# Performance work log

Hardware: AMD Instinct MI355X
Metric: run time of the kernel (lower is better)

Reference implementation:

```python
import jax, jax.numpy as jnp
import numpy as np

VOCAB, D = 50000, 300
B, LC = 64, 32
T, LT = 256, 64
N_SENTS = 5


def setup_inputs() -> dict:
    key = jax.random.key(0)
    k1, k2, k3 = jax.random.split(key, 3)
    claim = jax.random.randint(k1, (B, LC), 0, VOCAB)
    targets = jax.random.randint(k2, (B, T, LT), 0, VOCAB)
    embeddings = jax.random.normal(k3, (VOCAB, D), dtype=jnp.float32)
    return {"claim": claim, "targets": targets, "embeddings": embeddings, "n": N_SENTS}


def reference(claim, targets, embeddings, n):
    # Embedding lookups (frozen table)
    c = embeddings[claim]          # [B, Lc, d]
    t = embeddings[targets]        # [B, T, Lt, d]
    # batch_U = claim[:,None] @ targets^T  -> [B, T, Lc, Lt]
    U = jnp.einsum('bcd,btld->btcl', c, t)
    # softmax over target tokens (axis=3), max over claim tokens (axis=2)
    sm = jax.nn.softmax(U, axis=3)
    scores = jnp.max(sm, axis=2)           # [B, T, Lt]
    target_scores = jnp.sum(scores, axis=2)  # [B, T]
    # per-batch top-n target sentences (sorted order; torch used sorted=False,
    # the selected set is identical)
    _, idx = jax.lax.top_k(target_scores, n)  # [B, n]
    top = jnp.take_along_axis(U, idx[:, :, None, None], axis=1)  # [B, n, Lc, Lt]
    # L2-normalize over last axis (torch dim=2 of the [n, Lc, Lt] slice)
    norm = jnp.sqrt(jnp.sum(top * top, axis=3, keepdims=True))
    return top / norm
```

## Files before the change

### kernel.cpp

```cpp
#include <hip/hip_runtime.h>
#include <hip/hip_bf16.h>

#define VOCAB 50000
#define D     300
#define B_    64
#define LC    32
#define T_    256
#define LT    64
#define NSEL  5

#define A_U4   2560
#define A_HALF 20480
#define TROW   640

typedef _Float16 half8_t __attribute__((ext_vector_type(8)));
typedef float    f32x4   __attribute__((ext_vector_type(4)));

__global__ __launch_bounds__(256) void k_prep(const int* __restrict__ claim,
                                              const float* __restrict__ emb,
                                              _Float16* __restrict__ tab,
                                              _Float16* __restrict__ wsA,
                                              int tableBlocks) {
    int wave = threadIdx.x >> 6, lane = threadIdx.x & 63;
    if ((int)blockIdx.x < tableBlocks) {
        int r = blockIdx.x * 4 + wave;
        const float* src = emb + (size_t)r * D;
        _Float16* d = tab + (size_t)r * TROW;
#pragma unroll
        for (int i = 0; i < 5; ++i) {
            int k = lane + i * 64;
            float x = (k < D) ? src[k] : 0.0f;
            _Float16 h = (_Float16)x;
            int blk = k >> 5, off = k & 31;
            d[blk * 64 + off]      = h;
            d[blk * 64 + 32 + off] = (_Float16)(x - (float)h);
        }
    } else {
        int row = (blockIdx.x - tableBlocks) * 4 + wave;
        int b = row >> 5, m = row & 31;
        int tok = claim[row];
        const float* src = emb + (size_t)tok * D;
        _Float16* base = wsA + (size_t)b * A_HALF;
#pragma unroll
        for (int i = 0; i < 5; ++i) {
            int k = lane + i * 64;
            float x = (k < D) ? src[k] : 0.0f;
            _Float16 h = (_Float16)x;
            int sp = ((k >> 3) ^ (m & 7));
            int idx = (m * 40 + sp) * 8 + (k & 7);
            base[idx] = h;
            base[10240 + idx] = (_Float16)(x - (float)h);
        }
    }
}

__device__ __forceinline__ void split8(const float4& a, const float4& b,
                                       half8_t& hv, half8_t& lv) {
    float x[8] = {a.x, a.y, a.z, a.w, b.x, b.y, b.z, b.w};
#pragma unroll
    for (int i = 0; i < 8; ++i) {
        _Float16 h = (_Float16)x[i];
        hv[i] = h;
        lv[i] = (_Float16)(x[i] - (float)h);
    }
}

template<bool FAST, int NI>
__device__ __forceinline__ void compute_U(const uint4* sA,
                                          const float* __restrict__ emb,
                                          const _Float16* __restrict__ tab,
                                          const int* __restrict__ trow, int lcol0,
                                          int lane, f32x4 acc[2][NI]) {
    int ln = lane & 15, quad = lane >> 4;
#pragma unroll
    for (int mi = 0; mi < 2; ++mi)
#pragma unroll
        for (int ni = 0; ni < NI; ++ni) acc[mi][ni] = (f32x4)0.0f;

    int arow0 = ln * 40;
    int arow1 = (16 + ln) * 40;
    int key = ln & 7;
    int qo = quad * 8;

    if (FAST) {
        const _Float16* rp[NI];
#pragma unroll
        for (int ni = 0; ni < NI; ++ni) {
            int tok = trow[lcol0 + ni * 16 + ln];
            rp[ni] = tab + (size_t)tok * TROW;
        }
        half8_t bh[2][NI], bl[2][NI];
#pragma unroll
        for (int ni = 0; ni < NI; ++ni) {
            bh[0][ni] = *(const half8_t*)(rp[ni] + qo);
            bl[0][ni] = *(const half8_t*)(rp[ni] + 32 + qo);
        }
#pragma unroll
        for (int ks = 0; ks < 10; ++ks) {
            int cur = ks & 1, nxt = cur ^ 1;
            if (ks < 9) {
                int ko = (ks + 1) * 64 + qo;
#pragma unroll
                for (int ni = 0; ni < NI; ++ni) {
                    bh[nxt][ni] = *(const half8_t*)(rp[ni] + ko);
                    bl[nxt][ni] = *(const half8_t*)(rp[ni] + 32 + ko);
                }
            }
            int sp = (ks * 4 + quad) ^ key;
            half8_t ah[2], al[2];
            ah[0] = __builtin_bit_cast(half8_t, sA[arow0 + sp]);
            al[0] = __builtin_bit_cast(half8_t, sA[1280 + arow0 + sp]);
            ah[1] = __builtin_bit_cast(half8_t, sA[arow1 + sp]);
            al[1] = __builtin_bit_cast(half8_t, sA[1280 + arow1 + sp]);
#pragma unroll
            for (int mi = 0; mi < 2; ++mi)
#pragma unroll
                for (int ni = 0; ni < NI; ++ni) {
                    acc[mi][ni] = __builtin_amdgcn_mfma_f32_16x16x32_f16(ah[mi], bh[cur][ni], acc[mi][ni], 0, 0, 0);
                    acc[mi][ni] = __builtin_amdgcn_mfma_f32_16x16x32_f16(ah[mi], bl[cur][ni], acc[mi][ni], 0, 0, 0);
                    acc[mi][ni] = __builtin_amdgcn_mfma_f32_16x16x32_f16(al[mi], bh[cur][ni], acc[mi][ni], 0, 0, 0);
                }
        }
    } else {
        const float* bp[NI];
#pragma unroll
        for (int ni = 0; ni < NI; ++ni) {
            int tok = trow[lcol0 + ni * 16 + ln];
            bp[ni] = emb + (size_t)tok * D;
        }
#pragma unroll 1
        for (int ks = 0; ks < 10; ++ks) {
            int kb = ks * 32 + qo;
            int ka = kb > 296 ? 296 : kb;
            int kb4 = kb + 4;
            int kbb = kb4 > 296 ? 296 : kb4;
            float4 b0[NI], b1[NI];
#pragma unroll
            for (int ni = 0; ni < NI; ++ni) {
                b0[ni] = *(const float4*)(bp[ni] + ka);
                b1[ni] = *(const float4*)(bp[ni] + kbb);
            }
            if (kb >= 296) {
                float4 z = make_float4(0.f, 0.f, 0.f, 0.f);
#pragma unroll
                for (int ni = 0; ni < NI; ++ni) {
                    if (kb >= 300) b0[ni] = z;
                    b1[ni] = z;
                }
            }
            int sp = (ks * 4 + quad) ^ key;
            half8_t ah[2], al[2];
            ah[0] = __builtin_bit_cast(half8_t, sA[arow0 + sp]);
            al[0] = __builtin_bit_cast(half8_t, sA[1280 + arow0 + sp]);
            ah[1] = __builtin_bit_cast(half8_t, sA[arow1 + sp]);
            al[1] = __builtin_bit_cast(half8_t, sA[1280 + arow1 + sp]);
            half8_t bh[NI], bl[NI];
#pragma unroll
            for (int ni = 0; ni < NI; ++ni) split8(b0[ni], b1[ni], bh[ni], bl[ni]);
#pragma unroll
            for (int mi = 0; mi < 2; ++mi)
#pragma unroll
                for (int ni = 0; ni < NI; ++ni) {
                    acc[mi][ni] = __builtin_amdgcn_mfma_f32_16x16x32_f16(ah[mi], bh[ni], acc[mi][ni], 0, 0, 0);
                    acc[mi][ni] = __builtin_amdgcn_mfma_f32_16x16x32_f16(ah[mi], bl[ni], acc[mi][ni], 0, 0, 0);
                    acc[mi][ni] = __builtin_amdgcn_mfma_f32_16x16x32_f16(al[mi], bh[ni], acc[mi][ni], 0, 0, 0);
                }
        }
    }
}

__device__ __forceinline__ float xmax4(float v) {
    v = fmaxf(v, __shfl_xor(v, 1)); v = fmaxf(v, __shfl_xor(v, 2));
    v = fmaxf(v, __shfl_xor(v, 4)); v = fmaxf(v, __shfl_xor(v, 8));
    return v;
}
__device__ __forceinline__ float xsum4(float v) {
    v += __shfl_xor(v, 1); v += __shfl_xor(v, 2);
    v += __shfl_xor(v, 4); v += __shfl_xor(v, 8);
    return v;
}

template<bool FAST>
__global__ __launch_bounds__(256, 4) void k_scores(const int* __restrict__ targets,
                                                   const float* __restrict__ emb,
                                                   const _Float16* __restrict__ tab,
                                                   const _Float16* __restrict__ wsA,
                                                   float* __restrict__ wsScr) {
    __shared__ __align__(16) uint4 sA[A_U4];
    int wg = blockIdx.x;
    int xcd = wg & 7, rest = wg >> 3;
    int b = xcd * 8 + (rest >> 6);
    int tg = rest & 63;
    int tid = threadIdx.x;
    {
        const uint4* src = (const uint4*)(wsA + (size_t)b * A_HALF);
        for (int i = tid; i < A_U4; i += 256) sA[i] = src[i];
    }
    __syncthreads();

    int lane = tid & 63, wave = tid >> 6;
    int t = tg * 4 + wave;
    const int* trow = targets + ((size_t)b * T_ + t) * LT;

    f32x4 acc[2][4];
    compute_U<FAST, 4>(sA, emb, tab, trow, 0, lane, acc);

    float score_l[4] = {0.f, 0.f, 0.f, 0.f};
#pragma unroll
    for (int mi = 0; mi < 2; ++mi)
#pragma unroll
        for (int r = 0; r < 4; ++r) {
            float m = fmaxf(fmaxf(acc[mi][0][r], acc[mi][1][r]),
                            fmaxf(acc[mi][2][r], acc[mi][3][r]));
            m = xmax4(m);
            float p[4], s = 0.f;
#pragma unroll
            for (int ni = 0; ni < 4; ++ni) { p[ni] = __expf(acc[mi][ni][r] - m); s += p[ni]; }
            s = xsum4(s);
            float rv = 1.0f / s;
#pragma unroll
            for (int ni = 0; ni < 4; ++ni) score_l[ni] = fmaxf(score_l[ni], p[ni] * rv);
        }
    float tot = 0.f;
#pragma unroll
    for (int ni = 0; ni < 4; ++ni) {
        float v = score_l[ni];
        v = fmaxf(v, __shfl_xor(v, 16));
        v = fmaxf(v, __shfl_xor(v, 32));
        tot += v;
    }
    tot = xsum4(tot);
    if (lane == 0) wsScr[b * T_ + t] = tot;
}

template<bool FAST>
__global__ __launch_bounds__(256) void k_output(const int* __restrict__ targets,
                                                const float* __restrict__ emb,
                                                const _Float16* __restrict__ tab,
                                                const _Float16* __restrict__ wsA,
                                                const float* __restrict__ wsScr,
                                                float* __restrict__ out) {
    __shared__ __align__(16) uint4 sA[A_U4];
    __shared__ float sS[LC][4];
    __shared__ int sT;
    int b = blockIdx.y, j = blockIdx.x, tid = threadIdx.x;
    int lane = tid & 63, wave = tid >> 6;
    if (wave) {
        const uint4* src = (const uint4*)(wsA + (size_t)b * A_HALF);
        for (int i = tid - 64; i < A_U4; i += 192) sA[i] = src[i];
    } else {
        float v[4];
#pragma unroll
        for (int i = 0; i < 4; ++i) v[i] = wsScr[b * T_ + lane + 64 * i];
        int sel = 0;
        for (int r = 0; r <= j; ++r) {
            float bv = v[0]; int bi = lane;
#pragma unroll
            for (int i = 1; i < 4; ++i) {
                int idx = lane + 64 * i;
                if (v[i] > bv) { bv = v[i]; bi = idx; }
            }
            for (int off = 32; off > 0; off >>= 1) {
                float ov = __shfl_down(bv, off);
                int   oi = __shfl_down(bi, off);
                if (ov > bv || (ov == bv && oi < bi)) { bv = ov; bi = oi; }
            }
            bi = __shfl(bi, 0);
            sel = bi;
            if ((bi & 63) == lane) v[bi >> 6] = -1e30f;
        }
        if (lane == 0) sT = sel;
    }
    __syncthreads();

    int t = sT;
    const int* trow = targets + ((size_t)b * T_ + t) * LT;
    f32x4 acc[2][1];
    compute_U<FAST, 1>(sA, emb, tab, trow, wave * 16, lane, acc);

    int ln = lane & 15, quad = lane >> 4;
#pragma unroll
    for (int mi = 0; mi < 2; ++mi)
#pragma unroll
        for (int r = 0; r < 4; ++r) {
            float v = acc[mi][0][r] * acc[mi][0][r];
            v = xsum4(v);
            if (ln == 0) sS[mi * 16 + quad * 4 + r][wave] = v;
        }
    __syncthreads();

    float* obase = out + (size_t)(b * NSEL + j) * (LC * LT);
#pragma unroll
    for (int mi = 0; mi < 2; ++mi)
#pragma unroll
        for (int r = 0; r < 4; ++r) {
            int c = mi * 16 + quad * 4 + r;
            float ss = sS[c][0] + sS[c][1] + sS[c][2] + sS[c][3];
            float rinv = 1.0f / sqrtf(ss);
            obase[c * LT + wave * 16 + ln] = acc[mi][0][r] * rinv;
        }
}

extern "C" void kernel_launch(void* const* d_in, const int* in_sizes, int n_in,
                              void* d_out, int out_size, void* d_ws, size_t ws_size,
                              hipStream_t stream) {
    const int*   claim   = (const int*)d_in[0];
    const int*   targets = (const int*)d_in[1];
    const float* emb     = (const float*)d_in[2];

    const size_t tabBytes = (size_t)VOCAB * TROW * sizeof(_Float16);
    const size_t restBytes = (size_t)B_ * A_HALF * sizeof(_Float16)
                           + (size_t)B_ * T_ * sizeof(float)
                           + (size_t)B_ * NSEL * sizeof(int) + 256;
    bool fast = ws_size >= tabBytes + restBytes;

    char* p = (char*)d_ws;
    _Float16* tab = nullptr;
    if (fast) { tab = (_Float16*)p; p += tabBytes; }
    _Float16* wsA = (_Float16*)p; p += (size_t)B_ * A_HALF * sizeof(_Float16);
    float* wsScr = (float*)p;
    float* out   = (float*)d_out;

    int tableBlocks = fast ? (VOCAB / 4) : 0;
    k_prep<<<dim3(tableBlocks + 512), dim3(256), 0, stream>>>(claim, emb, tab, wsA, tableBlocks);
    if (fast) {
        k_scores<true><<<dim3(B_ * 64), dim3(256), 0, stream>>>(targets, emb, tab, wsA, wsScr);
        k_output<true><<<dim3(NSEL, B_), dim3(256), 0, stream>>>(targets, emb, tab, wsA, wsScr, out);
    } else {
        k_scores<false><<<dim3(B_ * 64), dim3(256), 0, stream>>>(targets, emb, tab, wsA, wsScr);
        k_output<false><<<dim3(NSEL, B_), dim3(256), 0, stream>>>(targets, emb, tab, wsA, wsScr, out);
    }
}
```

Before: 294.0 us.

## Drop the pre-split fp16 vocab table and build claim tiles in-kernel

Removes the prep kernel, which converted the whole 50000x300 embedding table into hi/lo fp16 pairs and staged claim tiles in workspace. Each scoring and output block now gathers its claim rows straight from the fp32 table, splits them into shared memory itself, and splits the target rows on the fly. This avoids writing and reading a roughly 64 MB converted table on every call. In exchange, target loads go back to fp32 with per-use conversion and no double buffering, and every block redoes the claim split.

```diff
diff --git a/kernel.cpp b/kernel.cpp
--- a/kernel.cpp
+++ b/kernel.cpp
@@ -1,5 +1,4 @@
 #include <hip/hip_runtime.h>
-#include <hip/hip_bf16.h>
 
 #define VOCAB 50000
 #define D     300
@@ -10,49 +9,10 @@
 #define NSEL  5
 
 #define A_U4   2560
-#define A_HALF 20480
-#define TROW   640
 
 typedef _Float16 half8_t __attribute__((ext_vector_type(8)));
 typedef float    f32x4   __attribute__((ext_vector_type(4)));
 
-__global__ __launch_bounds__(256) void k_prep(const int* __restrict__ claim,
-                                              const float* __restrict__ emb,
-                                              _Float16* __restrict__ tab,
-                                              _Float16* __restrict__ wsA,
-                                              int tableBlocks) {
-    int wave = threadIdx.x >> 6, lane = threadIdx.x & 63;
-    if ((int)blockIdx.x < tableBlocks) {
-        int r = blockIdx.x * 4 + wave;
-        const float* src = emb + (size_t)r * D;
-        _Float16* d = tab + (size_t)r * TROW;
-#pragma unroll
-        for (int i = 0; i < 5; ++i) {
-            int k = lane + i * 64;
-            float x = (k < D) ? src[k] : 0.0f;
-            _Float16 h = (_Float16)x;
-            int blk = k >> 5, off = k & 31;
-            d[blk * 64 + off]      = h;
-            d[blk * 64 + 32 + off] = (_Float16)(x - (float)h);
-        }
-    } else {
-        int row = (blockIdx.x - tableBlocks) * 4 + wave;
-        int b = row >> 5, m = row & 31;
-        int tok = claim[row];
-        const float* src = emb + (size_t)tok * D;
-        _Float16* base = wsA + (size_t)b * A_HALF;
-#pragma unroll
-        for (int i = 0; i < 5; ++i) {
-            int k = lane + i * 64;
-            float x = (k < D) ? src[k] : 0.0f;
-            _Float16 h = (_Float16)x;
-            int sp = ((k >> 3) ^ (m & 7));
-            int idx = (m * 40 + sp) * 8 + (k & 7);
-            base[idx] = h;
-            base[10240 + idx] = (_Float16)(x - (float)h);
-        }
-    }
-}
 
 __device__ __forceinline__ void split8(const float4& a, const float4& b,
                                        half8_t& hv, half8_t& lv) {
@@ -65,10 +25,48 @@
     }
 }
 
-template<bool FAST, int NI>
+__device__ __forceinline__ void build_sA(uint4* sA, const int* __restrict__ claim,
+                                         const float* __restrict__ emb,
+                                         int b, int tid) {
+    int m  = ((tid >> 6) << 3) + ((tid & 63) >> 3);
+    int c8 = tid & 7;
+    int tok = claim[b * LC + m];
+    const float* src = emb + (size_t)tok * D;
+    half8_t* h8 = (half8_t*)sA;
+#pragma unroll
+    for (int j = 0; j < 5; ++j) {
+        int s  = c8 * 5 + j;
+        int k0 = s * 8;
+        float x[8];
+        if (k0 <= 292) {
+            float4 a = *(const float4*)(src + k0);
+            float4 c = *(const float4*)(src + k0 + 4);
+            x[0]=a.x; x[1]=a.y; x[2]=a.z; x[3]=a.w;
+            x[4]=c.x; x[5]=c.y; x[6]=c.z; x[7]=c.w;
+        } else if (k0 == 296) {
+            float4 a = *(const float4*)(src + 296);
+            x[0]=a.x; x[1]=a.y; x[2]=a.z; x[3]=a.w;
+            x[4]=0.f; x[5]=0.f; x[6]=0.f; x[7]=0.f;
+        } else {
+#pragma unroll
+            for (int i = 0; i < 8; ++i) x[i] = 0.f;
+        }
+        half8_t hv, lv;
+#pragma unroll
+        for (int i = 0; i < 8; ++i) {
+            _Float16 h = (_Float16)x[i];
+            hv[i] = h;
+            lv[i] = (_Float16)(x[i] - (float)h);
+        }
+        int idx = m * 40 + (s ^ (m & 7));
+        h8[idx] = hv;
+        h8[1280 + idx] = lv;
+    }
+}
+
+template<int NI>
 __device__ __forceinline__ void compute_U(const uint4* sA,
                                           const float* __restrict__ emb,
-                                          const _Float16* __restrict__ tab,
                                           const int* __restrict__ trow, int lcol0,
                                           int lane, f32x4 acc[2][NI]) {
     int ln = lane & 15, quad = lane >> 4;
@@ -82,90 +80,49 @@
     int key = ln & 7;
     int qo = quad * 8;
 
-    if (FAST) {
-        const _Float16* rp[NI];
+    const float* bp[NI];
+#pragma unroll
+    for (int ni = 0; ni < NI; ++ni) {
+        int tok = trow[lcol0 + ni * 16 + ln];
+        bp[ni] = emb + (size_t)tok * D;
+    }
+#pragma unroll 1
+    for (int ks = 0; ks < 10; ++ks) {
+        int kb = ks * 32 + qo;
+        int ka = kb > 296 ? 296 : kb;
+        int kb4 = kb + 4;
+        int kbb = kb4 > 296 ? 296 : kb4;
+        float4 b0[NI], b1[NI];
 #pragma unroll
         for (int ni = 0; ni < NI; ++ni) {
-            int tok = trow[lcol0 + ni * 16 + ln];
-            rp[ni] = tab + (size_t)tok * TROW;
-        }
-        half8_t bh[2][NI], bl[2][NI];
-#pragma unroll
-        for (int ni = 0; ni < NI; ++ni) {
-            bh[0][ni] = *(const half8_t*)(rp[ni] + qo);
-            bl[0][ni] = *(const half8_t*)(rp[ni] + 32 + qo);
-        }
-#pragma unroll
-        for (int ks = 0; ks < 10; ++ks) {
-            int cur = ks & 1, nxt = cur ^ 1;
-            if (ks < 9) {
-                int ko = (ks + 1) * 64 + qo;
-#pragma unroll
-                for (int ni = 0; ni < NI; ++ni) {
-                    bh[nxt][ni] = *(const half8_t*)(rp[ni] + ko);
-                    bl[nxt][ni] = *(const half8_t*)(rp[ni] + 32 + ko);
-                }
-            }
-            int sp = (ks * 4 + quad) ^ key;
-            half8_t ah[2], al[2];
-            ah[0] = __builtin_bit_cast(half8_t, sA[arow0 + sp]);
-            al[0] = __builtin_bit_cast(half8_t, sA[1280 + arow0 + sp]);
-            ah[1] = __builtin_bit_cast(half8_t, sA[arow1 + sp]);
-            al[1] = __builtin_bit_cast(half8_t, sA[1280 + arow1 + sp]);
-#pragma unroll
-            for (int mi = 0; mi < 2; ++mi)
-#pragma unroll
-                for (int ni = 0; ni < NI; ++ni) {
-                    acc[mi][ni] = __builtin_amdgcn_mfma_f32_16x16x32_f16(ah[mi], bh[cur][ni], acc[mi][ni], 0, 0, 0);
-                    acc[mi][ni] = __builtin_amdgcn_mfma_f32_16x16x32_f16(ah[mi], bl[cur][ni], acc[mi][ni], 0, 0, 0);
-                    acc[mi][ni] = __builtin_amdgcn_mfma_f32_16x16x32_f16(al[mi], bh[cur][ni], acc[mi][ni], 0, 0, 0);
-                }
-        }
-    } else {
-        const float* bp[NI];
-#pragma unroll
-        for (int ni = 0; ni < NI; ++ni) {
-            int tok = trow[lcol0 + ni * 16 + ln];
-            bp[ni] = emb + (size_t)tok * D;
-        }
-#pragma unroll 1
-        for (int ks = 0; ks < 10; ++ks) {
-            int kb = ks * 32 + qo;
-            int ka = kb > 296 ? 296 : kb;
-            int kb4 = kb + 4;
-            int kbb = kb4 > 296 ? 296 : kb4;
-            float4 b0[NI], b1[NI];
+            b0[ni] = *(const float4*)(bp[ni] + ka);
+            b1[ni] = *(const float4*)(bp[ni] + kbb);
+        }
+        if (kb >= 296) {
+            float4 z = make_float4(0.f, 0.f, 0.f, 0.f);
 #pragma unroll
             for (int ni = 0; ni < NI; ++ni) {
-                b0[ni] = *(const float4*)(bp[ni] + ka);
-                b1[ni] = *(const float4*)(bp[ni] + kbb);
-            }
-            if (kb >= 296) {
-                float4 z = make_float4(0.f, 0.f, 0.f, 0.f);
-#pragma unroll
-                for (int ni = 0; ni < NI; ++ni) {
-                    if (kb >= 300) b0[ni] = z;
-                    b1[ni] = z;
-                }
-            }
-            int sp = (ks * 4 + quad) ^ key;
-            half8_t ah[2], al[2];
-            ah[0] = __builtin_bit_cast(half8_t, sA[arow0 + sp]);
-            al[0] = __builtin_bit_cast(half8_t, sA[1280 + arow0 + sp]);
-            ah[1] = __builtin_bit_cast(half8_t, sA[arow1 + sp]);
-            al[1] = __builtin_bit_cast(half8_t, sA[1280 + arow1 + sp]);
-            half8_t bh[NI], bl[NI];
-#pragma unroll
-            for (int ni = 0; ni < NI; ++ni) split8(b0[ni], b1[ni], bh[ni], bl[ni]);
-#pragma unroll
-            for (int mi = 0; mi < 2; ++mi)
-#pragma unroll
-                for (int ni = 0; ni < NI; ++ni) {
-                    acc[mi][ni] = __builtin_amdgcn_mfma_f32_16x16x32_f16(ah[mi], bh[ni], acc[mi][ni], 0, 0, 0);
-                    acc[mi][ni] = __builtin_amdgcn_mfma_f32_16x16x32_f16(ah[mi], bl[ni], acc[mi][ni], 0, 0, 0);
-                    acc[mi][ni] = __builtin_amdgcn_mfma_f32_16x16x32_f16(al[mi], bh[ni], acc[mi][ni], 0, 0, 0);
-                }
-        }
+                if (kb >= 300) b0[ni] = z;
+                b1[ni] = z;
+            }
+        }
+        int sp = (ks * 4 + quad) ^ key;
+        half8_t ah[2], al[2];
+        ah[0] = __builtin_bit_cast(half8_t, sA[arow0 + sp]);
+        al[0] = __builtin_bit_cast(half8_t, sA[1280 + arow0 + sp]);
+        ah[1] = __builtin_bit_cast(half8_t, sA[arow1 + sp]);
+        al[1] = __builtin_bit_cast(half8_t, sA[1280 + arow1 + sp]);
+        half8_t bh[NI], bl[NI];
+#pragma unroll
+        for (int ni = 0; ni < NI; ++ni) split8(b0[ni], b1[ni], bh[ni], bl[ni]);
+#pragma unroll
+        for (int mi = 0; mi < 2; ++mi)
+#pragma unroll
+            for (int ni = 0; ni < NI; ++ni) {
+                acc[mi][ni] = __builtin_amdgcn_mfma_f32_16x16x32_f16(ah[mi], bh[ni], acc[mi][ni], 0, 0, 0);
+                acc[mi][ni] = __builtin_amdgcn_mfma_f32_16x16x32_f16(ah[mi], bl[ni], acc[mi][ni], 0, 0, 0);
+                acc[mi][ni] = __builtin_amdgcn_mfma_f32_16x16x32_f16(al[mi], bh[ni], acc[mi][ni], 0, 0, 0);
+            }
     }
 }
 
@@ -180,11 +137,9 @@
     return v;
 }
 
-template<bool FAST>
-__global__ __launch_bounds__(256, 4) void k_scores(const int* __restrict__ targets,
+__global__ __launch_bounds__(256, 4) void k_scores(const int* __restrict__ claim,
+                                                   const int* __restrict__ targets,
                                                    const float* __restrict__ emb,
-                                                   const _Float16* __restrict__ tab,
-                                                   const _Float16* __restrict__ wsA,
                                                    float* __restrict__ wsScr) {
     __shared__ __align__(16) uint4 sA[A_U4];
     int wg = blockIdx.x;
@@ -192,10 +147,7 @@
     int b = xcd * 8 + (rest >> 6);
     int tg = rest & 63;
     int tid = threadIdx.x;
-    {
-        const uint4* src = (const uint4*)(wsA + (size_t)b * A_HALF);
-        for (int i = tid; i < A_U4; i += 256) sA[i] = src[i];
-    }
+    build_sA(sA, claim, emb, b, tid);
     __syncthreads();
 
     int lane = tid & 63, wave = tid >> 6;
@@ -203,7 +155,7 @@
     const int* trow = targets + ((size_t)b * T_ + t) * LT;
 
     f32x4 acc[2][4];
-    compute_U<FAST, 4>(sA, emb, tab, trow, 0, lane, acc);
+    compute_U<4>(sA, emb, trow, 0, lane, acc);
 
     float score_l[4] = {0.f, 0.f, 0.f, 0.f};
 #pragma unroll
@@ -233,11 +185,9 @@
     if (lane == 0) wsScr[b * T_ + t] = tot;
 }
 
-template<bool FAST>
-__global__ __launch_bounds__(256) void k_output(const int* __restrict__ targets,
+__global__ __launch_bounds__(256) void k_output(const int* __restrict__ claim,
+                                                const int* __restrict__ targets,
                                                 const float* __restrict__ emb,
-                                                const _Float16* __restrict__ tab,
-                                                const _Float16* __restrict__ wsA,
                                                 const float* __restrict__ wsScr,
                                                 float* __restrict__ out) {
     __shared__ __align__(16) uint4 sA[A_U4];
@@ -245,10 +195,8 @@
     __shared__ int sT;
     int b = blockIdx.y, j = blockIdx.x, tid = threadIdx.x;
     int lane = tid & 63, wave = tid >> 6;
-    if (wave) {
-        const uint4* src = (const uint4*)(wsA + (size_t)b * A_HALF);
-        for (int i = tid - 64; i < A_U4; i += 192) sA[i] = src[i];
-    } else {
+    build_sA(sA, claim, emb, b, tid);
+    if (wave == 0) {
         float v[4];
 #pragma unroll
         for (int i = 0; i < 4; ++i) v[i] = wsScr[b * T_ + lane + 64 * i];
@@ -276,7 +224,7 @@
     int t = sT;
     const int* trow = targets + ((size_t)b * T_ + t) * LT;
     f32x4 acc[2][1];
-    compute_U<FAST, 1>(sA, emb, tab, trow, wave * 16, lane, acc);
+    compute_U<1>(sA, emb, trow, wave * 16, lane, acc);
 
     int ln = lane & 15, quad = lane >> 4;
 #pragma unroll
@@ -308,26 +256,9 @@
     const int*   targets = (const int*)d_in[1];
     const float* emb     = (const float*)d_in[2];
 
-    const size_t tabBytes = (size_t)VOCAB * TROW * sizeof(_Float16);
-    const size_t restBytes = (size_t)B_ * A_HALF * sizeof(_Float16)
-                           + (size_t)B_ * T_ * sizeof(float)
-                           + (size_t)B_ * NSEL * sizeof(int) + 256;
-    bool fast = ws_size >= tabBytes + restBytes;
-
-    char* p = (char*)d_ws;
-    _Float16* tab = nullptr;
-    if (fast) { tab = (_Float16*)p; p += tabBytes; }
-    _Float16* wsA = (_Float16*)p; p += (size_t)B_ * A_HALF * sizeof(_Float16);
-    float* wsScr = (float*)p;
+    float* wsScr = (float*)d_ws;
     float* out   = (float*)d_out;
 
-    int tableBlocks = fast ? (VOCAB / 4) : 0;
-    k_prep<<<dim3(tableBlocks + 512), dim3(256), 0, stream>>>(claim, emb, tab, wsA, tableBlocks);
-    if (fast) {
-        k_scores<true><<<dim3(B_ * 64), dim3(256), 0, stream>>>(targets, emb, tab, wsA, wsScr);
-        k_output<true><<<dim3(NSEL, B_), dim3(256), 0, stream>>>(targets, emb, tab, wsA, wsScr, out);
-    } else {
-        k_scores<false><<<dim3(B_ * 64), dim3(256), 0, stream>>>(targets, emb, tab, wsA, wsScr);
-        k_output<false><<<dim3(NSEL, B_), dim3(256), 0, stream>>>(targets, emb, tab, wsA, wsScr, out);
-    }
-}
+    k_scores<<<dim3(B_ * 64), dim3(256), 0, stream>>>(claim, targets, emb, wsScr);
+    k_output<<<dim3(NSEL, B_), dim3(256), 0, stream>>>(claim, targets, emb, wsScr, out);
+}
```

Result: slower. 307.8 us (+4.7%).
